# Kernel optimization log

Measured on AMD Instinct MI355X. Metric: run time of the kernel, lower is better.

The kernel has to match this reference:

```python
import jax, jax.numpy as jnp
import numpy as np

B, NG, DEG, CW, OUT = 8, 16384, 16, 64, 256  # graphs, nodes/graph, avg degree, conv_width, output_dim


def _sage(x, src, dst, mask, Wl, bl, Wr):
    # PyG SAGEConv: mean-aggregate neighbors (src -> dst), lin_l(agg)+bias + lin_r(x)
    N = x.shape[0]
    s = jax.ops.segment_sum(x[src] * mask[:, None], dst, num_segments=N)
    c = jax.ops.segment_sum(mask, dst, num_segments=N)
    mean = s / jnp.maximum(c, 1.0)[:, None]
    return mean @ Wl.T + bl + x @ Wr.T


def _gcn(x, src, dst, mask, W, b):
    # PyG GCNConv: self-loops + symmetric deg^{-1/2} normalization; edge_weight == mask
    N = x.shape[0]
    xw = x @ W.T
    deg = 1.0 + jax.ops.segment_sum(mask, dst, num_segments=N)
    dis = jax.lax.rsqrt(deg)
    norm = dis[src] * mask * dis[dst]
    out = jax.ops.segment_sum(xw[src] * norm[:, None], dst, num_segments=N)
    return out + xw * (dis * dis)[:, None] + b


def _topk(x, src, dst, mask, w, n):
    # PyG TopKPooling: score = tanh(x.w/||w||), keep top ceil(0.5*n) per graph,
    # gate kept features by score, re-index edges (here: fixed-size edges + mask)
    score = jnp.tanh((x @ w) / jnp.linalg.norm(w))
    k = (n + 1) // 2
    vals, idx = jax.lax.top_k(score.reshape(B, n), k)  # [B,k], descending like PyG
    perm = (idx + (jnp.arange(B) * n)[:, None]).reshape(-1)  # global old indices
    x_new = x[perm] * vals.reshape(-1)[:, None]
    newpos = jnp.full((B * n,), -1, jnp.int32).at[perm].set(
        jnp.arange(B * k, dtype=jnp.int32))
    ns, nd = newpos[src], newpos[dst]
    m = mask * ((ns >= 0) & (nd >= 0)).astype(x.dtype)
    return x_new, jnp.maximum(ns, 0), jnp.maximum(nd, 0), m, k


def _readout(x, k):
    # [global_max_pool, global_mean_pool] per graph
    xr = x.reshape(B, k, -1)
    return jnp.concatenate([xr.max(axis=1), xr.mean(axis=1)], axis=1)


def setup_inputs() -> dict:
    key = jax.random.key(0)
    ks = jax.random.split(key, 24)
    N, Eg = B * NG, NG * DEG
    off = (jnp.arange(B) * NG)[:, None]
    src = (jax.random.randint(ks[0], (B, Eg), 0, NG) + off).reshape(-1)
    dst = (jax.random.randint(ks[1], (B, Eg), 0, NG) + off).reshape(-1)
    edge_index = jnp.stack([src, dst]).astype(jnp.int32)
    x = jax.random.normal(ks[2], (N, 2), jnp.float32)

    def xav(k, o, i):
        return jax.random.normal(k, (o, i), jnp.float32) * np.float32(np.sqrt(2.0 / (o + i)))

    def vec(k, d):
        return jax.random.normal(k, (d,), jnp.float32) * np.float32(1.0 / np.sqrt(d))

    return dict(
        x=x, edge_index=edge_index,
        Wl1=xav(ks[3], CW, 2), bl1=vec(ks[4], CW), Wr1=xav(ks[5], CW, 2),
        Wl2=xav(ks[6], CW, CW), bl2=vec(ks[7], CW), Wr2=xav(ks[8], CW, CW),
        W4=xav(ks[9], CW, CW), b4=vec(ks[10], CW),
        W5=xav(ks[11], CW, CW), b5=vec(ks[12], CW),
        wp1=vec(ks[13], CW), wp2=vec(ks[14], CW), wp4=vec(ks[15], CW), wp5=vec(ks[16], CW),
        Wa=xav(ks[17], 128, 2 * CW), ba=vec(ks[18], 128),
        Wb=xav(ks[19], 64, 128), bb=vec(ks[20], 64),
        Wc=xav(ks[21], OUT, 64), bc=vec(ks[22], OUT),
    )


def reference(x, edge_index, Wl1, bl1, Wr1, Wl2, bl2, Wr2, W4, b4, W5, b5,
              wp1, wp2, wp4, wp5, Wa, ba, Wb, bb, Wc, bc):
    src, dst = edge_index[0], edge_index[1]
    mask = jnp.ones(src.shape[0], x.dtype)
    n = NG
    h = jax.nn.relu(_sage(x, src, dst, mask, Wl1, bl1, Wr1))
    h, src, dst, mask, n = _topk(h, src, dst, mask, wp1, n)
    x1 = _readout(h, n)
    h = jax.nn.relu(_sage(h, src, dst, mask, Wl2, bl2, Wr2))
    h, src, dst, mask, n = _topk(h, src, dst, mask, wp2, n)
    x2 = _readout(h, n)
    h = jax.nn.relu(_gcn(h, src, dst, mask, W4, b4))
    h, src, dst, mask, n = _topk(h, src, dst, mask, wp4, n)
    x4 = _readout(h, n)
    h = jax.nn.relu(_gcn(h, src, dst, mask, W5, b5))
    h, src, dst, mask, n = _topk(h, src, dst, mask, wp5, n)
    x5 = _readout(h, n)
    z = x1 + x2 + x4 + x5  # [B, 2*CW]
    z = jax.nn.relu(z @ Wa.T + ba)
    z = jax.nn.relu(z @ Wb.T + bb)
    z = z @ Wc.T + bc
    return jax.nn.softmax(z, axis=1)
```

## Files before the change

kernel.cpp:

```cpp
#include <hip/hip_runtime.h>
#include <math.h>

constexpr int Bq  = 8;
constexpr int NGq = 16384;
constexpr int Nq  = Bq * NGq;
constexpr int Eq  = Nq * 16;
constexpr int Eg  = Eq / 8;

__global__ void k_prep(const float* __restrict__ Wl2, const float* __restrict__ Wr2,
                       const float* __restrict__ W4, const float* __restrict__ W5,
                       const float* __restrict__ Wa, const float* __restrict__ Wb,
                       const float* __restrict__ Wc,
                       const float* __restrict__ w1, const float* __restrict__ w2,
                       const float* __restrict__ w4p, const float* __restrict__ w5p,
                       float* __restrict__ wT, float* __restrict__ wMT,
                       float* __restrict__ winv, int* __restrict__ bsum) {
    int t = threadIdx.x, b = blockIdx.x;
    if (b < 4) {
        const float* in = (b == 0) ? Wl2 : (b == 1) ? Wr2 : (b == 2) ? W4 : W5;
        float* out = wT + (size_t)b * 4096;
        for (int i = t; i < 4096; i += 256) {
            int r = i >> 6, c = i & 63;
            out[c * 64 + r] = in[r * 64 + c];
        }
    } else if (b == 4) {
        float* WaT = wMT;
        for (int i = t; i < 16384; i += 256) {
            int r = i >> 7, c = i & 127;
            WaT[c * 128 + r] = Wa[r * 128 + c];
        }
    } else if (b == 5) {
        float* WbT = wMT + 16384;
        for (int i = t; i < 8192; i += 256) {
            int r = i >> 7, c = i & 127;
            WbT[c * 64 + r] = Wb[r * 128 + c];
        }
    } else if (b == 6) {
        float* WcT = wMT + 16384 + 8192;
        for (int i = t; i < 16384; i += 256) {
            int r = i >> 6, c = i & 63;
            WcT[c * 256 + r] = Wc[r * 64 + c];
        }
    } else {
        int vsel = t >> 6, lane = t & 63;
        const float* wp = (vsel == 0) ? w1 : (vsel == 1) ? w2 : (vsel == 2) ? w4p : w5p;
        float v = wp[lane];
        float ww = v * v;
        for (int o = 32; o; o >>= 1) ww += __shfl_xor(ww, o);
        if (lane == 0) winv[vsel] = 1.0f / sqrtf(ww);
        for (int i = t; i < 512; i += 256) bsum[i] = 0;
    }
}

__global__ void k_bcnt(const int* __restrict__ dst, int* __restrict__ bcnt) {
    __shared__ int hist[512];
    int t = threadIdx.x;
    int blk = blockIdx.x;
    if (t < 512) hist[t] = 0;
    __syncthreads();
    int e0 = blk * 8192;
#pragma unroll
    for (int i = 0; i < 8; i++) {
        int e = e0 + i * 1024 + t;
        atomicAdd(&hist[dst[e] >> 8], 1);
    }
    __syncthreads();
    if (t < 512) { int h = hist[t]; if (h) atomicAdd(&bcnt[t], h); }
}

__global__ void k_scan_b2(int* __restrict__ bsum, int* __restrict__ bcur) {
    __shared__ int s[512];
    int t = threadIdx.x;
    int own = bsum[t];
    s[t] = own;
    __syncthreads();
    for (int d = 1; d < 512; d <<= 1) {
        int v = (t >= d) ? s[t - d] : 0;
        __syncthreads();
        if (t >= d) s[t] += v;
        __syncthreads();
    }
    int ex = s[t] - own;
    bsum[t] = ex;
    bcur[t] = ex;
}

__global__ void k_csr_a(const int* __restrict__ src, const int* __restrict__ dst,
                        int* __restrict__ bcur, unsigned* __restrict__ pairs) {
    __shared__ int hist[512];
    __shared__ int base[512];
    __shared__ int lcur[512];
    int t = threadIdx.x;
    int blk = blockIdx.x;
    int e0 = blk * 8192;
    int bk[8]; unsigned p[8];
#pragma unroll
    for (int i = 0; i < 8; i++) {
        int e = e0 + i * 1024 + t;
        int d = dst[e];
        bk[i] = d >> 8;
        p[i] = ((unsigned)(d & 255) << 24) | (unsigned)src[e];
    }
    if (t < 512) hist[t] = 0;
    __syncthreads();
#pragma unroll
    for (int i = 0; i < 8; i++) atomicAdd(&hist[bk[i]], 1);
    __syncthreads();
    if (t < 512) {
        int h = hist[t];
        base[t] = h ? atomicAdd(&bcur[t], h) : 0;
        lcur[t] = 0;
    }
    __syncthreads();
#pragma unroll
    for (int i = 0; i < 8; i++) {
        int b = bk[i];
        int r = atomicAdd(&lcur[b], 1);
        pairs[base[b] + r] = p[i];
    }
}

__global__ void k_csr_b(const int* __restrict__ bsum, const unsigned* __restrict__ pairs,
                        const float2* __restrict__ x2,
                        int* __restrict__ off, int* __restrict__ csrc,
                        float2* __restrict__ mean) {
    __shared__ int lcnt[256];
    __shared__ int lcur[256];
    __shared__ int wsum[4];
    int b = blockIdx.x, t = threadIdx.x;
    int beg = bsum[b];
    int end = (b < 511) ? bsum[b + 1] : Eq;
    lcnt[t] = 0;
    __syncthreads();
    for (int i = beg + t; i < end; i += 256)
        atomicAdd(&lcnt[pairs[i] >> 24], 1);
    __syncthreads();
    int v = lcnt[t];
    int lane = t & 63, wv = t >> 6;
    int val = v;
    for (int o = 1; o < 64; o <<= 1) {
        int u = __shfl_up(val, o);
        if (lane >= o) val += u;
    }
    if (lane == 63) wsum[wv] = val;
    __syncthreads();
    int add = 0;
    for (int q = 0; q < wv; q++) add += wsum[q];
    int gpos = beg + val + add - v;
    off[b * 256 + t] = gpos;
    lcur[t] = gpos;
    if (b == 511 && t == 255) off[Nq] = Eq;
    __syncthreads();
    for (int i = beg + t; i < end; i += 256) {
        unsigned p = pairs[i];
        int pos = atomicAdd(&lcur[p >> 24], 1);
        csrc[pos] = (int)(p & 0x00FFFFFFu);
    }
    __syncthreads();
    float s0 = 0.f, s1 = 0.f;
    for (int e = gpos; e < gpos + v; e++) {
        float2 xv = x2[csrc[e]];
        s0 += xv.x; s1 += xv.y;
    }
    float c = fmaxf((float)v, 1.0f);
    mean[b * 256 + t] = make_float2(s0 / c, s1 / c);
}

__global__ void k_sage1e(const float* __restrict__ x, const float2* __restrict__ mean,
                         const float* __restrict__ Wl, const float* __restrict__ bl,
                         const float* __restrict__ Wr, const float* __restrict__ wp,
                         const float* __restrict__ invn,
                         float* __restrict__ out, float* __restrict__ score) {
    int blk = blockIdx.x;
    int g = blk & 7, i = blk >> 3;
    int wv = threadIdx.x >> 6, j = threadIdx.x & 63;
    int n = g * NGq + i * 4 + wv;
    float2 xn = ((const float2*)x)[n];
    float2 m = mean[n];
    float2 wl = ((const float2*)Wl)[j];
    float2 wr = ((const float2*)Wr)[j];
    float v = wl.x * m.x + wl.y * m.y + bl[j] + wr.x * xn.x + wr.y * xn.y;
    v = fmaxf(v, 0.f);
    out[n * 64 + j] = v;
    float d = v * wp[j];
    for (int o = 32; o; o >>= 1) d += __shfl_xor(d, o);
    if (j == 0) score[n] = d * invn[0];
}

template<int NM>
__global__ __launch_bounds__(256, 2)
void k_linf(const float* __restrict__ h, const float* __restrict__ WaT,
            const float* __restrict__ WbT, const float* __restrict__ bias,
            float* __restrict__ oa, float* __restrict__ ob, int Nn, int linB,
            const int* __restrict__ off, const int* __restrict__ csrc,
            const int* __restrict__ map, const int* __restrict__ orig,
            float* __restrict__ dis, int ng, int disB,
            const float* __restrict__ hr, float* __restrict__ part, int kk, int G) {
    __shared__ float smx[256], ssm[256];
    int blk = blockIdx.x;
    if (blk < linB) {
        int j = threadIdx.x & 63, wv = threadIdx.x >> 6;
        float wa[64];
        float wb[NM == 2 ? 64 : 1];
#pragma unroll
        for (int q = 0; q < 64; q++) wa[q] = WaT[q * 64 + j];
        if constexpr (NM == 2) {
#pragma unroll
            for (int q = 0; q < 64; q++) wb[q] = WbT[q * 64 + j];
        }
        float bj = 0.f;
        if constexpr (NM == 2) bj = bias[j];
        int stride = linB * 4;
        for (int n = blk * 4 + wv; n < Nn; n += stride) {
            float iv = h[(size_t)n * 64 + j];
            float acca = 0.f;
            float accb = bj;
#pragma unroll
            for (int q = 0; q < 64; q++) {
                float s = __int_as_float(__builtin_amdgcn_readlane(__float_as_int(iv), q));
                acca += s * wa[q];
                if constexpr (NM == 2) accb += s * wb[q];
            }
            oa[(size_t)n * 64 + j] = acca;
            if constexpr (NM == 2) ob[(size_t)n * 64 + j] = accb;
        }
    } else if (blk < linB + disB) {
        int b2 = blk - linB;
        int g = b2 & 7, i = b2 >> 3;
        int wv = threadIdx.x >> 6, j = threadIdx.x & 63;
        int n = g * ng + i * 4 + wv;
        int o = orig[n];
        int beg = off[o], end = off[o + 1];
        int c = 0;
        for (int base = beg; base < end; base += 64) {
            int d = end - base; if (d > 64) d = 64;
            int cs = (j < d) ? map[csrc[base + j]] : -1;
            c += __popcll(__ballot(cs >= 0));
        }
        if (j == 0) dis[n] = 1.0f / sqrtf(1.0f + (float)c);
    } else {
        int b3 = blk - linB - disB;
        int b = b3 & 7, g = b3 >> 3;
        int rows = kk / G;
        int t = threadIdx.x, j = t & 63, q = t >> 6;
        const float* basep = hr + ((size_t)b * kk + (size_t)g * rows) * 64;
        float mx = -3.0e38f, sm = 0.f;
        for (int i = q; i < rows; i += 4) {
            float v = basep[i * 64 + j];
            mx = fmaxf(mx, v); sm += v;
        }
        smx[t] = mx; ssm[t] = sm;
        __syncthreads();
        if (q == 0) {
            for (int r = 1; r < 4; r++) { mx = fmaxf(mx, smx[j + 64 * r]); sm += ssm[j + 64 * r]; }
            part[(b * G + g) * 128 + j] = mx;
            part[(b * G + g) * 128 + 64 + j] = sm;
        }
    }
}

__global__ void k_readout_part(const float* __restrict__ h, float* __restrict__ part,
                               int k, int G) {
    __shared__ float smx[256], ssm[256];
    int blk = blockIdx.x;
    int b = blk & 7, g = blk >> 3;
    int rows = k / G;
    int t = threadIdx.x, j = t & 63, q = t >> 6;
    const float* basep = h + ((size_t)b * k + (size_t)g * rows) * 64;
    float mx = -3.0e38f, sm = 0.f;
    for (int i = q; i < rows; i += 4) {
        float v = basep[i * 64 + j];
        mx = fmaxf(mx, v); sm += v;
    }
    smx[t] = mx; ssm[t] = sm;
    __syncthreads();
    if (q == 0) {
        for (int r = 1; r < 4; r++) { mx = fmaxf(mx, smx[j + 64 * r]); sm += ssm[j + 64 * r]; }
        part[(b * G + g) * 128 + j] = mx;
        part[(b * G + g) * 128 + 64 + j] = sm;
    }
}

__global__ void k_zfin(const float* __restrict__ part, float* __restrict__ z) {
    __shared__ float red[8][128];
    int b = blockIdx.x, t = threadIdx.x;
    int j = t & 127, s = t >> 7;
    const float* p; int g0;
    if (s < 4)       { p = part + (size_t)(b * 64) * 128;           g0 = s * 16; }
    else if (s < 6)  { p = part + 65536 + (size_t)(b * 32) * 128;   g0 = (s - 4) * 16; }
    else if (s == 6) { p = part + 98304 + (size_t)(b * 16) * 128;   g0 = 0; }
    else             { p = part + 114688 + (size_t)(b * 16) * 128;  g0 = 0; }
    float accm = -3.0e38f, accs = 0.f;
    for (int g = g0; g < g0 + 16; g++) {
        float v = p[g * 128 + j];
        accm = fmaxf(accm, v);
        accs += v;
    }
    red[s][j] = (j < 64) ? accm : accs;
    __syncthreads();
    if (s == 0) {
        float zv;
        if (j < 64) {
            float m1 = fmaxf(fmaxf(red[0][j], red[1][j]), fmaxf(red[2][j], red[3][j]));
            float m2 = fmaxf(red[4][j], red[5][j]);
            zv = m1 + m2 + red[6][j] + red[7][j];
        } else {
            float s1 = red[0][j] + red[1][j] + red[2][j] + red[3][j];
            float s2 = red[4][j] + red[5][j];
            zv = s1 / 8192.0f + s2 / 4096.0f + red[6][j] / 2048.0f + red[7][j] / 1024.0f;
        }
        z[b * 128 + j] = zv;
    }
}

template<int M>
__global__ void k_topk(float* __restrict__ score, int* __restrict__ newpos,
                       int* __restrict__ perm, int* __restrict__ map, int mode) {
    constexpr int n = M * 1024;
    constexpr int k = n / 2;
    __shared__ unsigned hist[256];
    __shared__ unsigned sh_pfx, sh_msk, sh_rem;
    __shared__ int sh_eqtot, sh_ctr;
    __shared__ int wtot[16];
    __shared__ int runTie, runGt;
    int t = threadIdx.x, b = blockIdx.x;
    int base = b * n;
    int lane = t & 63, wv = t >> 6;

    unsigned kr[M];
#pragma unroll
    for (int i = 0; i < M; i++) {
        unsigned u = __float_as_uint(score[base + t + (i << 10)]);
        kr[i] = u ^ ((u >> 31) ? 0xFFFFFFFFu : 0x80000000u);
    }
    if (t < 256) hist[t] = 0;
    if (t == 0) { sh_pfx = 0; sh_msk = 0; sh_rem = (unsigned)k;
                  sh_eqtot = 0; sh_ctr = 0; runTie = 0; runGt = 0; }
    __syncthreads();

    for (int shift = 24; shift >= 0; shift -= 8) {
        unsigned pfx = sh_pfx, msk = sh_msk;
#pragma unroll
        for (int i = 0; i < M; i++)
            if ((kr[i] & msk) == pfx) atomicAdd(&hist[(kr[i] >> shift) & 255], 1u);
        __syncthreads();
        if (t < 64) {
            unsigned rem = sh_rem;
            unsigned c0 = hist[255 - (t * 4 + 0)];
            unsigned c1 = hist[255 - (t * 4 + 1)];
            unsigned c2 = hist[255 - (t * 4 + 2)];
            unsigned c3 = hist[255 - (t * 4 + 3)];
            unsigned s = c0 + c1 + c2 + c3;
            unsigned sc = s;
            for (int o = 1; o < 64; o <<= 1) {
                unsigned u = __shfl_up(sc, o);
                if (t >= o) sc += u;
            }
            unsigned run = sc - s;
            unsigned cc[4] = {c0, c1, c2, c3};
#pragma unroll
            for (int q = 0; q < 4; q++) {
                unsigned incl = run + cc[q];
                if (run < rem && incl >= rem) {
                    int bb = 255 - (t * 4 + q);
                    sh_rem = rem - run;
                    sh_pfx = pfx | ((unsigned)bb << shift);
                    sh_msk = msk | (255u << shift);
                }
                run = incl;
            }
        }
        __syncthreads();
        if (t < 256) hist[t] = 0;
        __syncthreads();
    }
    unsigned K = sh_pfx;
    int T = (int)sh_rem;

    int le = 0;
#pragma unroll
    for (int i = 0; i < M; i++) le += (kr[i] == K) ? 1 : 0;
    for (int o = 32; o; o >>= 1) le += __shfl_xor(le, o);
    if (lane == 0) atomicAdd(&sh_eqtot, le);
    __syncthreads();

    if (sh_eqtot == T) {
#pragma unroll
        for (int i = 0; i < M; i++) {
            int cur = base + t + (i << 10);
            bool kept = kr[i] >= K;
            unsigned long long mk = __ballot(kept);
            int pos = 0;
            if (mk) {
                int fl = __ffsll(mk) - 1;
                int bp = 0;
                if (lane == fl) bp = atomicAdd(&sh_ctr, __popcll(mk));
                bp = __shfl(bp, fl);
                pos = bp + __popcll(mk & ((1ull << lane) - 1ull));
            }
            if (kept && pos < k) {
                newpos[cur] = b * k + pos;
                perm[b * k + pos] = cur;
                unsigned ob = (kr[i] & 0x80000000u) ? (kr[i] ^ 0x80000000u) : ~kr[i];
                score[cur] = tanhf(__uint_as_float(ob));
            } else newpos[cur] = -1;
        }
    } else {
        for (int i = 0; i < M; i++) {
            unsigned key = kr[i];
            int gt = key > K ? 1 : 0;
            int eq = key == K ? 1 : 0;
            int val = (eq << 16) | gt;
            for (int o = 1; o < 64; o <<= 1) {
                int v = __shfl_up(val, o);
                if (lane >= o) val += v;
            }
            if (lane == 63) wtot[wv] = val;
            __syncthreads();
            int add = 0;
            for (int q = 0; q < 16; q++) if (q < wv) add += wtot[q];
            val += add;
            int eqIncl = val >> 16, gtIncl = val & 0xffff;
            int eqExcl = eqIncl - eq, gtExcl = gtIncl - gt;
            int kept = gt | (eq & ((runTie + eqExcl) < T ? 1 : 0));
            int cur = base + t + (i << 10);
            if (kept) {
                int selEqBefore = runTie + eqExcl; if (selEqBefore > T) selEqBefore = T;
                int nl = runGt + gtExcl + selEqBefore;
                if (nl < k) {
                    newpos[cur] = b * k + nl;
                    perm[b * k + nl] = cur;
                    unsigned ob = (key & 0x80000000u) ? (key ^ 0x80000000u) : ~key;
                    score[cur] = tanhf(__uint_as_float(ob));
                } else newpos[cur] = -1;
            } else newpos[cur] = -1;
            __syncthreads();
            if (t == 1023) { runTie += eqIncl; runGt += gtIncl; }
            __syncthreads();
        }
    }

    if (mode) {
        __syncthreads();
        int gbase = b * NGq;
        for (int i2 = t; i2 < NGq; i2 += 1024) {
            int gi = gbase + i2;
            if (mode == 1) map[gi] = newpos[gi];
            else { int m = map[gi]; map[gi] = (m >= 0) ? newpos[m] : -1; }
        }
    }
}

__global__ void k_compact(const float* __restrict__ hin, const float* __restrict__ score,
                          const int* __restrict__ perm, const int* __restrict__ orig_in,
                          int* __restrict__ orig_out, int first,
                          float* __restrict__ hout, int k) {
    int blk = blockIdx.x;
    int g = blk & 7, i = blk >> 3;
    int wv = threadIdx.x >> 6, j = threadIdx.x & 63;
    int nn = g * k + i * 4 + wv;
    int old = perm[nn];
    hout[nn * 64 + j] = hin[old * 64 + j] * score[old];
    if (j == 0) orig_out[nn] = first ? old : orig_in[old];
}

__global__ void k_sage_gather2(const float* __restrict__ gl, const int* __restrict__ off,
                               const int* __restrict__ csrc, const int* __restrict__ map,
                               const int* __restrict__ orig, const float* __restrict__ wp,
                               const float* __restrict__ invn,
                               float* __restrict__ out, float* __restrict__ score, int ng) {
    int blk = blockIdx.x;
    int g = blk & 7, i = blk >> 3;
    int wv = threadIdx.x >> 6, l = threadIdx.x & 63;
    int n = g * ng + i * 4 + wv;
    int o = orig[n];
    int beg = off[o], end = off[o + 1];
    int fg = l & 15, es = l >> 4;
    float4 own = make_float4(0.f, 0.f, 0.f, 0.f);
    if (es == 0) own = ((const float4*)(out + (size_t)n * 64))[fg];
    float4 acc = make_float4(0.f, 0.f, 0.f, 0.f);
    int cnt = 0;
    for (int base = beg; base < end; base += 64) {
        int d = end - base; if (d > 64) d = 64;
        int cs = (l < d) ? map[csrc[base + l]] : -1;
        cnt += __popcll(__ballot(cs >= 0));
        for (int e = 0; e < d; e += 4) {
            int c = __shfl(cs, e + es);
            if (c >= 0) {
                float4 v = ((const float4*)(gl + (size_t)c * 64))[fg];
                acc.x += v.x; acc.y += v.y; acc.z += v.z; acc.w += v.w;
            }
        }
    }
    acc.x += __shfl_xor(acc.x, 16); acc.y += __shfl_xor(acc.y, 16);
    acc.z += __shfl_xor(acc.z, 16); acc.w += __shfl_xor(acc.w, 16);
    acc.x += __shfl_xor(acc.x, 32); acc.y += __shfl_xor(acc.y, 32);
    acc.z += __shfl_xor(acc.z, 32); acc.w += __shfl_xor(acc.w, 32);
    float c = fmaxf((float)cnt, 1.0f);
    float4 v;
    v.x = fmaxf(acc.x / c + own.x, 0.f);
    v.y = fmaxf(acc.y / c + own.y, 0.f);
    v.z = fmaxf(acc.z / c + own.z, 0.f);
    v.w = fmaxf(acc.w / c + own.w, 0.f);
    float dsc = 0.f;
    if (es == 0) {
        ((float4*)(out + (size_t)n * 64))[fg] = v;
        float4 w4 = ((const float4*)wp)[fg];
        dsc = v.x * w4.x + v.y * w4.y + v.z * w4.z + v.w * w4.w;
    }
    for (int o2 = 32; o2; o2 >>= 1) dsc += __shfl_xor(dsc, o2);
    if (l == 0) score[n] = dsc * invn[0];
}

__global__ void k_gcn_gather(const float* __restrict__ xw, const int* __restrict__ off,
                             const int* __restrict__ csrc, const int* __restrict__ map,
                             const int* __restrict__ orig, const float* __restrict__ dis,
                             const float* __restrict__ bb, const float* __restrict__ wp,
                             const float* __restrict__ invn,
                             float* __restrict__ out, float* __restrict__ score, int ng) {
    int blk = blockIdx.x;
    int g = blk & 7, i = blk >> 3;
    int wv = threadIdx.x >> 6, l = threadIdx.x & 63;
    int n = g * ng + i * 4 + wv;
    int o = orig[n];
    int beg = off[o], end = off[o + 1];
    int fg = l & 15, es = l >> 4;
    float dn = dis[n];
    float4 own = make_float4(0.f, 0.f, 0.f, 0.f);
    if (es == 0) own = ((const float4*)(xw + (size_t)n * 64))[fg];
    float4 acc = make_float4(0.f, 0.f, 0.f, 0.f);
    for (int base = beg; base < end; base += 64) {
        int d = end - base; if (d > 64) d = 64;
        int cs = -1; float dsv = 0.f;
        if (l < d) {
            int cc = map[csrc[base + l]];
            if (cc >= 0) { cs = cc; dsv = dis[cc]; }
        }
        for (int e = 0; e < d; e += 4) {
            int c = __shfl(cs, e + es);
            float dv = __shfl(dsv, e + es);
            if (c >= 0) {
                float4 v = ((const float4*)(xw + (size_t)c * 64))[fg];
                acc.x += v.x * dv; acc.y += v.y * dv;
                acc.z += v.z * dv; acc.w += v.w * dv;
            }
        }
    }
    acc.x += __shfl_xor(acc.x, 16); acc.y += __shfl_xor(acc.y, 16);
    acc.z += __shfl_xor(acc.z, 16); acc.w += __shfl_xor(acc.w, 16);
    acc.x += __shfl_xor(acc.x, 32); acc.y += __shfl_xor(acc.y, 32);
    acc.z += __shfl_xor(acc.z, 32); acc.w += __shfl_xor(acc.w, 32);
    float dsc = 0.f;
    if (es == 0) {
        float4 b4 = ((const float4*)bb)[fg];
        float dd = dn * dn;
        float4 v;
        v.x = fmaxf(acc.x * dn + own.x * dd + b4.x, 0.f);
        v.y = fmaxf(acc.y * dn + own.y * dd + b4.y, 0.f);
        v.z = fmaxf(acc.z * dn + own.z * dd + b4.z, 0.f);
        v.w = fmaxf(acc.w * dn + own.w * dd + b4.w, 0.f);
        ((float4*)(out + (size_t)n * 64))[fg] = v;
        float4 w4 = ((const float4*)wp)[fg];
        dsc = v.x * w4.x + v.y * w4.y + v.z * w4.z + v.w * w4.w;
    }
    for (int o2 = 32; o2; o2 >>= 1) dsc += __shfl_xor(dsc, o2);
    if (l == 0) score[n] = dsc * invn[0];
}

__global__ void k_mlp(const float* __restrict__ z,
                      const float* __restrict__ WaT, const float* __restrict__ ba,
                      const float* __restrict__ WbT, const float* __restrict__ bb,
                      const float* __restrict__ WcT, const float* __restrict__ bc,
                      float* __restrict__ out) {
    __shared__ float sz[128];
    __shared__ float sa[128];
    __shared__ float sb2[64];
    __shared__ float sc[256];
    __shared__ float tmp[256];
    __shared__ float wred[4];
    int b = blockIdx.x, t = threadIdx.x;
    if (t < 128) sz[t] = z[b * 128 + t];
    __syncthreads();
    {
        int o = t & 127, half = t >> 7;
        float v = 0.f;
        int q0 = half * 64;
        for (int q = q0; q < q0 + 64; q++) v += sz[q] * WaT[q * 128 + o];
        tmp[t] = v;
        __syncthreads();
        if (t < 128) sa[t] = fmaxf(tmp[t] + tmp[t + 128] + ba[t], 0.f);
        __syncthreads();
    }
    {
        int o = t & 63, qr = t >> 6;
        float v = 0.f;
        int q0 = qr * 32;
        for (int q = q0; q < q0 + 32; q++) v += sa[q] * WbT[q * 64 + o];
        tmp[t] = v;
        __syncthreads();
        if (t < 64) sb2[t] = fmaxf(tmp[t] + tmp[t + 64] + tmp[t + 128] + tmp[t + 192] + bb[t], 0.f);
        __syncthreads();
    }
    {
        float v = bc[t];
        for (int q = 0; q < 64; q++) v += sb2[q] * WcT[q * 256 + t];
        sc[t] = v;
    }
    __syncthreads();
    float m = sc[t];
    for (int o2 = 32; o2; o2 >>= 1) m = fmaxf(m, __shfl_xor(m, o2));
    if ((t & 63) == 0) wred[t >> 6] = m;
    __syncthreads();
    m = fmaxf(fmaxf(wred[0], wred[1]), fmaxf(wred[2], wred[3]));
    __syncthreads();
    float e = expf(sc[t] - m);
    float s = e;
    for (int o2 = 32; o2; o2 >>= 1) s += __shfl_xor(s, o2);
    if ((t & 63) == 0) wred[t >> 6] = s;
    __syncthreads();
    s = wred[0] + wred[1] + wred[2] + wred[3];
    out[b * 256 + t] = e / s;
}

extern "C" void kernel_launch(void* const* d_in, const int* in_sizes, int n_in,
                              void* d_out, int out_size, void* d_ws, size_t ws_size,
                              hipStream_t stream) {
    const float* x   = (const float*)d_in[0];
    const int*   ei  = (const int*)d_in[1];
    const int* src = ei;
    const int* dst = ei + Eq;
    const float* Wl1 = (const float*)d_in[2];
    const float* bl1 = (const float*)d_in[3];
    const float* Wr1 = (const float*)d_in[4];
    const float* Wl2 = (const float*)d_in[5];
    const float* bl2 = (const float*)d_in[6];
    const float* Wr2 = (const float*)d_in[7];
    const float* W4  = (const float*)d_in[8];
    const float* b4  = (const float*)d_in[9];
    const float* W5  = (const float*)d_in[10];
    const float* b5  = (const float*)d_in[11];
    const float* wp1 = (const float*)d_in[12];
    const float* wp2 = (const float*)d_in[13];
    const float* wp4 = (const float*)d_in[14];
    const float* wp5 = (const float*)d_in[15];
    const float* Wa  = (const float*)d_in[16];
    const float* ba  = (const float*)d_in[17];
    const float* Wb  = (const float*)d_in[18];
    const float* bbv = (const float*)d_in[19];
    const float* Wc  = (const float*)d_in[20];
    const float* bc  = (const float*)d_in[21];
    float* out = (float*)d_out;

    const int N1 = Nq / 2, N2 = Nq / 4, N3 = Nq / 8, N4 = Nq / 16;

    char* w = (char*)d_ws;
    float* hA    = (float*)w; w += (size_t)Nq * 64 * 4;
    float* hB    = (float*)w; w += (size_t)N1 * 64 * 4;
    int*   csrc  = (int*)w;   w += (size_t)Eq * 4;
    int*   coff  = (int*)w;   w += (size_t)(Nq + 1) * 4;
    int*   bcur  = (int*)w;   w += (size_t)Nq * 4;
    int*   cnt   = (int*)w;   w += (size_t)Nq * 4;
    float* dis   = (float*)w; w += (size_t)Nq * 4;
    float* score = (float*)w; w += (size_t)Nq * 4;
    int*   newpos= (int*)w;   w += (size_t)Nq * 4;
    int*   map   = (int*)w;   w += (size_t)Nq * 4;
    int*   perm  = (int*)w;   w += (size_t)Nq * 4;
    int*   origA = (int*)w;   w += (size_t)Nq * 4;
    int*   origB = (int*)w;   w += (size_t)Nq * 4;
    int*   bsum  = (int*)w;   w += 512 * 4;
    float* part  = (float*)w; w += (size_t)131072 * 4;
    float* z     = (float*)w; w += 1024 * 4;
    float* wT    = (float*)w; w += 4 * 4096 * 4;
    float* wMT   = (float*)w; w += (16384 + 8192 + 16384) * 4;
    float* WlT2 = wT, *WrT2 = wT + 4096, *W4T = wT + 8192, *W5T = wT + 12288;
    float* WaT = wMT, *WbT = wMT + 16384, *WcT = wMT + 16384 + 8192;
    float* gl = hA + (size_t)N1 * 64;
    unsigned* pairs = (unsigned*)hA;
    float2* mean = (float2*)cnt;
    float* winv = (float*)(bcur + 1024);

    k_prep<<<8, 256, 0, stream>>>(Wl2, Wr2, W4, W5, Wa, Wb, Wc,
                                  wp1, wp2, wp4, wp5, wT, wMT, winv, bsum);
    k_bcnt<<<256, 1024, 0, stream>>>(dst, bsum);
    k_scan_b2<<<1, 512, 0, stream>>>(bsum, bcur);
    k_csr_a<<<256, 1024, 0, stream>>>(src, dst, bcur, pairs);
    k_csr_b<<<512, 256, 0, stream>>>(bsum, pairs, (const float2*)x, coff, csrc, mean);

    k_sage1e<<<Nq / 4, 256, 0, stream>>>(x, mean, Wl1, bl1, Wr1, wp1, winv, hA, score);
    k_topk<16><<<8, 1024, 0, stream>>>(score, newpos, perm, map, 1);
    k_compact<<<N1 / 4, 256, 0, stream>>>(hA, score, perm, nullptr, origA, 1, hB, N1 / 8);

    k_linf<2><<<1024 + 512, 256, 0, stream>>>(hB, WlT2, WrT2, bl2, gl, hA, N1, 1024,
                                              nullptr, nullptr, nullptr, nullptr,
                                              nullptr, 0, 0,
                                              hB, part, NGq / 2, 64);
    k_sage_gather2<<<N1 / 4, 256, 0, stream>>>(gl, coff, csrc, map, origA,
                                               wp2, winv + 1, hA, score, N1 / 8);
    k_topk<8><<<8, 1024, 0, stream>>>(score, newpos, perm, map, 2);
    k_compact<<<N2 / 4, 256, 0, stream>>>(hA, score, perm, origA, origB, 0, hB, N2 / 8);

    k_linf<1><<<512 + 8192 + 256, 256, 0, stream>>>(hB, W4T, nullptr, nullptr, hA, nullptr,
                                                    N2, 512,
                                                    coff, csrc, map, origB, dis, N2 / 8, 8192,
                                                    hB, part + 65536, NGq / 4, 32);
    k_gcn_gather<<<N2 / 4, 256, 0, stream>>>(hA, coff, csrc, map, origB, dis,
                                             b4, wp4, winv + 2,
                                             hA + (size_t)N2 * 64, score, N2 / 8);
    k_topk<4><<<8, 1024, 0, stream>>>(score, newpos, perm, map, 2);
    k_compact<<<N3 / 4, 256, 0, stream>>>(hA + (size_t)N2 * 64, score, perm,
                                          origB, origA, 0, hB, N3 / 8);

    k_linf<1><<<256 + 4096 + 128, 256, 0, stream>>>(hB, W5T, nullptr, nullptr, hA, nullptr,
                                                    N3, 256,
                                                    coff, csrc, map, origA, dis, N3 / 8, 4096,
                                                    hB, part + 98304, NGq / 8, 16);
    k_gcn_gather<<<N3 / 4, 256, 0, stream>>>(hA, coff, csrc, map, origA, dis,
                                             b5, wp5, winv + 3,
                                             hA + (size_t)N3 * 64, score, N3 / 8);
    k_topk<2><<<8, 1024, 0, stream>>>(score, newpos, perm, map, 0);
    k_compact<<<N4 / 4, 256, 0, stream>>>(hA + (size_t)N3 * 64, score, perm,
                                          origA, origB, 0, hB, N4 / 8);

    k_readout_part<<<8 * 16, 256, 0, stream>>>(hB, part + 114688, NGq / 16, 16);
    k_zfin<<<8, 1024, 0, stream>>>(part, z);
    k_mlp<<<8, 256, 0, stream>>>(z, WaT, ba, WbT, bbv, WcT, bc, out);
}
```

Before: 447.2 us.

## Fuse top-k compaction into consumers via perm-indexed gathers

Removes the separate k_compact kernels that materialized gated, compacted feature rows after each top-k. Consumers (linear, readout) now read the uncompacted features through perm and multiply by the score inline, and top-k writes the orig index mapping directly. This saves four launches and one full write/read of the pooled features per stage, at the cost of scattered row gathers in the linear and readout kernels and an extra buffer.

Result: no change. 452.7 us (+1.2%).

```diff
diff --git a/kernel.cpp b/kernel.cpp
--- a/kernel.cpp
+++ b/kernel.cpp
@@ -189,13 +189,15 @@
 
 template<int NM>
 __global__ __launch_bounds__(256, 2)
-void k_linf(const float* __restrict__ h, const float* __restrict__ WaT,
-            const float* __restrict__ WbT, const float* __restrict__ bias,
+void k_linf(const float* __restrict__ h, const int* __restrict__ perm,
+            const float* __restrict__ score,
+            const float* __restrict__ WaT, const float* __restrict__ WbT,
+            const float* __restrict__ bias,
             float* __restrict__ oa, float* __restrict__ ob, int Nn, int linB,
             const int* __restrict__ off, const int* __restrict__ csrc,
             const int* __restrict__ map, const int* __restrict__ orig,
             float* __restrict__ dis, int ng, int disB,
-            const float* __restrict__ hr, float* __restrict__ part, int kk, int G) {
+            float* __restrict__ part, int kk, int G) {
     __shared__ float smx[256], ssm[256];
     int blk = blockIdx.x;
     if (blk < linB) {
@@ -212,7 +214,9 @@
         if constexpr (NM == 2) bj = bias[j];
         int stride = linB * 4;
         for (int n = blk * 4 + wv; n < Nn; n += stride) {
-            float iv = h[(size_t)n * 64 + j];
+            int p = perm[n];
+            float sc = score[p];
+            float iv = h[(size_t)p * 64 + j] * sc;
             float acca = 0.f;
             float accb = bj;
 #pragma unroll
@@ -243,10 +247,11 @@
         int b = b3 & 7, g = b3 >> 3;
         int rows = kk / G;
         int t = threadIdx.x, j = t & 63, q = t >> 6;
-        const float* basep = hr + ((size_t)b * kk + (size_t)g * rows) * 64;
+        const int* pb = perm + b * kk + g * rows;
         float mx = -3.0e38f, sm = 0.f;
         for (int i = q; i < rows; i += 4) {
-            float v = basep[i * 64 + j];
+            int row = pb[i];
+            float v = h[(size_t)row * 64 + j] * score[row];
             mx = fmaxf(mx, v); sm += v;
         }
         smx[t] = mx; ssm[t] = sm;
@@ -259,17 +264,19 @@
     }
 }
 
-__global__ void k_readout_part(const float* __restrict__ h, float* __restrict__ part,
-                               int k, int G) {
+__global__ void k_readout_part(const float* __restrict__ h, const int* __restrict__ perm,
+                               const float* __restrict__ score,
+                               float* __restrict__ part, int k, int G) {
     __shared__ float smx[256], ssm[256];
     int blk = blockIdx.x;
     int b = blk & 7, g = blk >> 3;
     int rows = k / G;
     int t = threadIdx.x, j = t & 63, q = t >> 6;
-    const float* basep = h + ((size_t)b * k + (size_t)g * rows) * 64;
+    const int* pb = perm + b * k + g * rows;
     float mx = -3.0e38f, sm = 0.f;
     for (int i = q; i < rows; i += 4) {
-        float v = basep[i * 64 + j];
+        int row = pb[i];
+        float v = h[(size_t)row * 64 + j] * score[row];
         mx = fmaxf(mx, v); sm += v;
     }
     smx[t] = mx; ssm[t] = sm;
@@ -315,7 +322,9 @@
 
 template<int M>
 __global__ void k_topk(float* __restrict__ score, int* __restrict__ newpos,
-                       int* __restrict__ perm, int* __restrict__ map, int mode) {
+                       int* __restrict__ perm, int* __restrict__ map, int mode,
+                       const int* __restrict__ orig_in, int* __restrict__ orig_out,
+                       int og) {
     constexpr int n = M * 1024;
     constexpr int k = n / 2;
     __shared__ unsigned hist[256];
@@ -401,6 +410,7 @@
             if (kept && pos < k) {
                 newpos[cur] = b * k + pos;
                 perm[b * k + pos] = cur;
+                if (og) orig_out[b * k + pos] = (og == 1) ? cur : orig_in[cur];
                 unsigned ob = (kr[i] & 0x80000000u) ? (kr[i] ^ 0x80000000u) : ~kr[i];
                 score[cur] = tanhf(__uint_as_float(ob));
             } else newpos[cur] = -1;
@@ -430,6 +440,7 @@
                 if (nl < k) {
                     newpos[cur] = b * k + nl;
                     perm[b * k + nl] = cur;
+                    if (og) orig_out[b * k + nl] = (og == 1) ? cur : orig_in[cur];
                     unsigned ob = (key & 0x80000000u) ? (key ^ 0x80000000u) : ~key;
                     score[cur] = tanhf(__uint_as_float(ob));
                 } else newpos[cur] = -1;
@@ -449,19 +460,6 @@
             else { int m = map[gi]; map[gi] = (m >= 0) ? newpos[m] : -1; }
         }
     }
-}
-
-__global__ void k_compact(const float* __restrict__ hin, const float* __restrict__ score,
-                          const int* __restrict__ perm, const int* __restrict__ orig_in,
-                          int* __restrict__ orig_out, int first,
-                          float* __restrict__ hout, int k) {
-    int blk = blockIdx.x;
-    int g = blk & 7, i = blk >> 3;
-    int wv = threadIdx.x >> 6, j = threadIdx.x & 63;
-    int nn = g * k + i * 4 + wv;
-    int old = perm[nn];
-    hout[nn * 64 + j] = hin[old * 64 + j] * score[old];
-    if (j == 0) orig_out[nn] = first ? old : orig_in[old];
 }
 
 __global__ void k_sage_gather2(const float* __restrict__ gl, const int* __restrict__ off,
@@ -656,6 +654,7 @@
     char* w = (char*)d_ws;
     float* hA    = (float*)w; w += (size_t)Nq * 64 * 4;
     float* hB    = (float*)w; w += (size_t)N1 * 64 * 4;
+    float* hC    = (float*)w; w += (size_t)N1 * 64 * 4;
     int*   csrc  = (int*)w;   w += (size_t)Eq * 4;
     int*   coff  = (int*)w;   w += (size_t)(Nq + 1) * 4;
     int*   bcur  = (int*)w;   w += (size_t)Nq * 4;
@@ -674,7 +673,6 @@
     float* wMT   = (float*)w; w += (16384 + 8192 + 16384) * 4;
     float* WlT2 = wT, *WrT2 = wT + 4096, *W4T = wT + 8192, *W5T = wT + 12288;
     float* WaT = wMT, *WbT = wMT + 16384, *WcT = wMT + 16384 + 8192;
-    float* gl = hA + (size_t)N1 * 64;
     unsigned* pairs = (unsigned*)hA;
     float2* mean = (float2*)cnt;
     float* winv = (float*)(bcur + 1024);
@@ -687,41 +685,34 @@
     k_csr_b<<<512, 256, 0, stream>>>(bsum, pairs, (const float2*)x, coff, csrc, mean);
 
     k_sage1e<<<Nq / 4, 256, 0, stream>>>(x, mean, Wl1, bl1, Wr1, wp1, winv, hA, score);
-    k_topk<16><<<8, 1024, 0, stream>>>(score, newpos, perm, map, 1);
-    k_compact<<<N1 / 4, 256, 0, stream>>>(hA, score, perm, nullptr, origA, 1, hB, N1 / 8);
-
-    k_linf<2><<<1024 + 512, 256, 0, stream>>>(hB, WlT2, WrT2, bl2, gl, hA, N1, 1024,
+    k_topk<16><<<8, 1024, 0, stream>>>(score, newpos, perm, map, 1, nullptr, origA, 1);
+
+    k_linf<2><<<1024 + 512, 256, 0, stream>>>(hA, perm, score, WlT2, WrT2, bl2,
+                                              hC, hB, N1, 1024,
                                               nullptr, nullptr, nullptr, nullptr,
                                               nullptr, 0, 0,
-                                              hB, part, NGq / 2, 64);
-    k_sage_gather2<<<N1 / 4, 256, 0, stream>>>(gl, coff, csrc, map, origA,
-                                               wp2, winv + 1, hA, score, N1 / 8);
-    k_topk<8><<<8, 1024, 0, stream>>>(score, newpos, perm, map, 2);
-    k_compact<<<N2 / 4, 256, 0, stream>>>(hA, score, perm, origA, origB, 0, hB, N2 / 8);
-
-    k_linf<1><<<512 + 8192 + 256, 256, 0, stream>>>(hB, W4T, nullptr, nullptr, hA, nullptr,
-                                                    N2, 512,
+                                              part, NGq / 2, 64);
+    k_sage_gather2<<<N1 / 4, 256, 0, stream>>>(hC, coff, csrc, map, origA,
+                                               wp2, winv + 1, hB, score, N1 / 8);
+    k_topk<8><<<8, 1024, 0, stream>>>(score, newpos, perm, map, 2, origA, origB, 2);
+
+    k_linf<1><<<512 + 8192 + 256, 256, 0, stream>>>(hB, perm, score, W4T, nullptr, nullptr,
+                                                    hC, nullptr, N2, 512,
                                                     coff, csrc, map, origB, dis, N2 / 8, 8192,
-                                                    hB, part + 65536, NGq / 4, 32);
-    k_gcn_gather<<<N2 / 4, 256, 0, stream>>>(hA, coff, csrc, map, origB, dis,
-                                             b4, wp4, winv + 2,
-                                             hA + (size_t)N2 * 64, score, N2 / 8);
-    k_topk<4><<<8, 1024, 0, stream>>>(score, newpos, perm, map, 2);
-    k_compact<<<N3 / 4, 256, 0, stream>>>(hA + (size_t)N2 * 64, score, perm,
-                                          origB, origA, 0, hB, N3 / 8);
-
-    k_linf<1><<<256 + 4096 + 128, 256, 0, stream>>>(hB, W5T, nullptr, nullptr, hA, nullptr,
-                                                    N3, 256,
+                                                    part + 65536, NGq / 4, 32);
+    k_gcn_gather<<<N2 / 4, 256, 0, stream>>>(hC, coff, csrc, map, origB, dis,
+                                             b4, wp4, winv + 2, hB, score, N2 / 8);
+    k_topk<4><<<8, 1024, 0, stream>>>(score, newpos, perm, map, 2, origB, origA, 2);
+
+    k_linf<1><<<256 + 4096 + 128, 256, 0, stream>>>(hB, perm, score, W5T, nullptr, nullptr,
+                                                    hC, nullptr, N3, 256,
                                                     coff, csrc, map, origA, dis, N3 / 8, 4096,
-                                                    hB, part + 98304, NGq / 8, 16);
-    k_gcn_gather<<<N3 / 4, 256, 0, stream>>>(hA, coff, csrc, map, origA, dis,
-                                             b5, wp5, winv + 3,
-                                             hA + (size_t)N3 * 64, score, N3 / 8);
-    k_topk<2><<<8, 1024, 0, stream>>>(score, newpos, perm, map, 0);
-    k_compact<<<N4 / 4, 256, 0, stream>>>(hA + (size_t)N3 * 64, score, perm,
-                                          origA, origB, 0, hB, N4 / 8);
-
-    k_readout_part<<<8 * 16, 256, 0, stream>>>(hB, part + 114688, NGq / 16, 16);
+                                                    part + 98304, NGq / 8, 16);
+    k_gcn_gather<<<N3 / 4, 256, 0, stream>>>(hC, coff, csrc, map, origA, dis,
+                                             b5, wp5, winv + 3, hB, score, N3 / 8);
+    k_topk<2><<<8, 1024, 0, stream>>>(score, newpos, perm, map, 0, nullptr, nullptr, 0);
+
+    k_readout_part<<<8 * 16, 256, 0, stream>>>(hB, perm, score, part + 114688, NGq / 16, 16);
     k_zfin<<<8, 1024, 0, stream>>>(part, z);
     k_mlp<<<8, 256, 0, stream>>>(z, WaT, ba, WbT, bbv, WcT, bc, out);
 }
```
